# Kernel optimization log

Measured on AMD Instinct MI355X. Metric: run time of the kernel, lower is better.

## Reference

```python
import jax, jax.numpy as jnp
import numpy as np

D, E, K, H = 512, 8, 2, 128   # input_dim, num_experts, top-k, expert hidden (Expert default)
CAPF = 1.25                    # capacity_factor
N = 32768                      # tokens


def setup_inputs() -> dict:
    key = jax.random.key(0)
    ks = jax.random.split(key, 6)
    s = 0.02
    return {
        "x":  jax.random.normal(ks[0], (N, D), jnp.float32),
        "Wr": jax.random.normal(ks[1], (D, E), jnp.float32) * s,   # router linear weight
        "br": jnp.zeros((E,), jnp.float32),
        "W1": jax.random.normal(ks[2], (E, D, H), jnp.float32) * s,  # expert first linear (stacked)
        "b1": jnp.zeros((E, H), jnp.float32),
        "W2": jax.random.normal(ks[3], (E, H, D), jnp.float32) * s,  # expert second linear (stacked)
        "b2": jnp.zeros((E, D), jnp.float32),
    }


def reference(x, Wr, br, W1, b1, W2, b2):
    n = x.shape[0]
    # ---- router (eval mode: no noise, temperature=1) ----
    logits = x @ Wr + br                                   # [N, E]
    topk_vals, topk_idx = jax.lax.top_k(logits, K)         # [N, K]
    gates_k = jax.nn.softmax(topk_vals, axis=-1)
    rows = jnp.arange(n)[:, None]
    sparse_gates = jnp.zeros_like(logits).at[rows, topk_idx].set(gates_k)  # [N, E]
    confidence = topk_vals.max(axis=-1).mean()
    # ---- capacity-limited dispatch (keep first `cap` routed tokens per expert) ----
    cap = int(CAPF * (n / E))
    mask = sparse_gates > 0                                # [N, E] routed mask
    pos = jnp.cumsum(mask, axis=0) - 1                     # rank of token within expert queue
    keep = mask & (pos < cap)                              # [N, E]
    load = keep.sum(axis=0).astype(x.dtype)                # [E]
    # ---- per-expert 2-layer FFN over all tokens, combined with keep mask ----
    # (original adds expert output un-weighted by gates to kept token positions)
    h = jax.nn.relu(jnp.einsum('nd,edh->enh', x, W1) + b1[:, None, :])   # [E, N, H]
    y = jnp.einsum('enh,ehd->end', h, W2) + b2[:, None, :]               # [E, N, D]
    out = jnp.einsum('ne,end->nd', keep.astype(x.dtype), y)             # [N, D]
    # ---- load-balance stats ----
    load_dist = load / (load.sum() + 1e-8)
    load_loss = (load_dist * jnp.log(load_dist + 1e-8)).sum()
    return out, load_loss, load_dist, confidence
```

## Files before the change

kernel.cpp:

```cpp
#include <hip/hip_runtime.h>

#define D 512
#define E 8
#define H 128
#define BM 128
#define HP 136
#define RT 8

typedef __attribute__((ext_vector_type(8))) short short8v;
typedef __attribute__((ext_vector_type(4))) short short4v;
typedef __attribute__((ext_vector_type(4))) float float4v;

__device__ inline short f2bf(float f) {
  union { float f; unsigned u; } v; v.f = f;
  unsigned r = v.u + 0x7fffu + ((v.u >> 16) & 1u);
  return (short)(r >> 16);
}
__device__ inline float bf2f(short s) {
  union { unsigned u; float f; } v;
  v.u = ((unsigned)(unsigned short)s) << 16;
  return v.f;
}
__device__ inline void gload_lds4(const void* g, void* l) {
  __builtin_amdgcn_global_load_lds(
      (const __attribute__((address_space(1))) unsigned int*)g,
      (__attribute__((address_space(3))) unsigned int*)l, 4, 0, 0);
}

__global__ void k_swizzle(const float* __restrict__ W1, const float* __restrict__ W2,
                          short* __restrict__ W1f, short* __restrict__ W2f) {
  const int e = blockIdx.y;
  const int lane = threadIdx.x & 63;
  const int wv = threadIdx.x >> 6;
  const int r = lane & 15, g = lane >> 4;
  const int which = blockIdx.x >> 4;
  const int fbase = ((blockIdx.x & 15) * 4 + wv) * 2;
  if (which == 0) {
#pragma unroll
    for (int f = fbase; f < fbase + 2; ++f) {
      int ks = f >> 3, t = f & 7;
      const float* src = W1 + ((size_t)e * D + ks * 32 + g * 8) * H + t * 16 + r;
      short8v o;
#pragma unroll
      for (int j = 0; j < 8; ++j) o[j] = f2bf(src[(size_t)j * H]);
      *(short8v*)(W1f + (((size_t)e * 128 + f) * 64 + lane) * 8) = o;
    }
  } else {
#pragma unroll
    for (int f = fbase; f < fbase + 2; ++f) {
      int t = f >> 2, ks = f & 3;
      const float* src = W2 + ((size_t)e * H + ks * 32 + g * 8) * D + t * 16 + r;
      short8v o;
#pragma unroll
      for (int j = 0; j < 8; ++j) o[j] = f2bf(src[(size_t)j * D]);
      *(short8v*)(W2f + (((size_t)e * 128 + f) * 64 + lane) * 8) = o;
    }
  }
}

__global__ void k_router(const float* __restrict__ x, const float* __restrict__ Wr,
                         const float* __restrict__ br, int* __restrict__ tokE,
                         float* __restrict__ confPart, short* __restrict__ xb) {
  const int lane = threadIdx.x & 63;
  const int wave = threadIdx.x >> 6;
  const int tbase = (blockIdx.x * 4 + wave) * RT;

  float wr[8][8];
  const float4* wrp = reinterpret_cast<const float4*>(Wr) + lane * 16;
#pragma unroll
  for (int j = 0; j < 8; ++j) {
    float4 a = wrp[j * 2 + 0];
    float4 b = wrp[j * 2 + 1];
    wr[j][0] = a.x; wr[j][1] = a.y; wr[j][2] = a.z; wr[j][3] = a.w;
    wr[j][4] = b.x; wr[j][5] = b.y; wr[j][6] = b.z; wr[j][7] = b.w;
  }

  const int myE = ((lane & 1) << 2) | (lane & 2) | ((lane >> 2) & 1);
  const float brv = br[myE];

  float conf = 0.f;

#pragma unroll 2
  for (int tt = 0; tt < RT; ++tt) {
    const int token = tbase + tt;
    const float4* xp = reinterpret_cast<const float4*>(x + (size_t)token * D + lane * 8);
    float4 x0 = xp[0], x1 = xp[1];
    float xv[8] = {x0.x, x0.y, x0.z, x0.w, x1.x, x1.y, x1.z, x1.w};

    if (xb) {
      short8v p;
#pragma unroll
      for (int j = 0; j < 8; ++j) p[j] = f2bf(xv[j]);
      *(short8v*)(xb + (size_t)token * D + lane * 8) = p;
    }

    float v[8] = {0, 0, 0, 0, 0, 0, 0, 0};
#pragma unroll
    for (int j = 0; j < 8; ++j)
#pragma unroll
      for (int e = 0; e < E; ++e)
        v[e] += xv[j] * wr[j][e];

#pragma unroll
    for (int i = 0; i < 4; ++i) {
      float a = v[i] + __shfl_xor(v[i], 1, 64);
      float b = v[i + 4] + __shfl_xor(v[i + 4], 1, 64);
      v[i] = (lane & 1) ? b : a;
    }
#pragma unroll
    for (int i = 0; i < 2; ++i) {
      float a = v[i] + __shfl_xor(v[i], 2, 64);
      float b = v[i + 2] + __shfl_xor(v[i + 2], 2, 64);
      v[i] = (lane & 2) ? b : a;
    }
    {
      float a = v[0] + __shfl_xor(v[0], 4, 64);
      float b = v[1] + __shfl_xor(v[1], 4, 64);
      v[0] = (lane & 4) ? b : a;
    }
    v[0] += __shfl_xor(v[0], 8, 64);
    v[0] += __shfl_xor(v[0], 16, 64);
    v[0] += __shfl_xor(v[0], 32, 64);

    const float logit = v[0] + brv;

    float m1 = logit; int i1 = myE;
#pragma unroll
    for (int m = 1; m <= 4; m <<= 1) {
      float om = __shfl_xor(m1, m, 64);
      int oi = __shfl_xor(i1, m, 64);
      bool take = (om > m1) || (om == m1 && oi < i1);
      m1 = take ? om : m1;
      i1 = take ? oi : i1;
    }
    float s1 = (myE == i1) ? -1e30f : logit; int j1 = myE;
#pragma unroll
    for (int m = 1; m <= 4; m <<= 1) {
      float om = __shfl_xor(s1, m, 64);
      int oi = __shfl_xor(j1, m, 64);
      bool take = (om > s1) || (om == s1 && oi < j1);
      s1 = take ? om : s1;
      j1 = take ? oi : j1;
    }

    if (lane == 0) {
      tokE[token * 2 + 0] = i1;
      tokE[token * 2 + 1] = j1;
    }
    conf += m1;
  }

  __shared__ float cf[4];
  if (lane == 0) cf[wave] = conf;
  __syncthreads();
  if (threadIdx.x == 0) confPart[blockIdx.x] = cf[0] + cf[1] + cf[2] + cf[3];
}

__global__ void k_count(const int* __restrict__ tokE, int* __restrict__ chunkCnt) {
  __shared__ int c[E];
  if (threadIdx.x < E) c[threadIdx.x] = 0;
  __syncthreads();
  int token = blockIdx.x * 256 + threadIdx.x;
  atomicAdd(&c[tokE[token * 2 + 0]], 1);
  atomicAdd(&c[tokE[token * 2 + 1]], 1);
  __syncthreads();
  if (threadIdx.x < E) chunkCnt[blockIdx.x * E + threadIdx.x] = c[threadIdx.x];
}

__global__ void k_scan(const int* __restrict__ chunkCnt, const float* __restrict__ confPart,
                       int* __restrict__ chunkOff, int* __restrict__ kept,
                       float* __restrict__ outTail, int nConf, int cap, int nTok) {
  const int lane = threadIdx.x & 63;
  const int e = threadIdx.x >> 6;
  __shared__ int keptS[E];

  int v0 = chunkCnt[lane * E + e];
  int v1 = chunkCnt[(64 + lane) * E + e];
  int s0 = v0, s1 = v1;
#pragma unroll
  for (int off = 1; off < 64; off <<= 1) {
    int t0 = __shfl_up(s0, off, 64);
    int t1 = __shfl_up(s1, off, 64);
    if (lane >= off) { s0 += t0; s1 += t1; }
  }
  int tot0 = __shfl(s0, 63, 64);
  int total = tot0 + __shfl(s1, 63, 64);
  chunkOff[lane * E + e] = s0 - v0;
  chunkOff[(64 + lane) * E + e] = tot0 + s1 - v1;
  if (lane == 0) {
    int k = min(total, cap);
    kept[e] = k;
    keptS[e] = k;
  }

  __shared__ float s[512];
  float a = 0.f;
  for (int i = threadIdx.x; i < nConf; i += 512) a += confPart[i];
  s[threadIdx.x] = a;
  __syncthreads();
  for (int st = 256; st > 0; st >>= 1) {
    if (threadIdx.x < st) s[threadIdx.x] += s[threadIdx.x + st];
    __syncthreads();
  }
  if (threadIdx.x == 0) {
    float tot = 0.f, ld[E];
    for (int i = 0; i < E; ++i) { ld[i] = (float)keptS[i]; tot += ld[i]; }
    float denom = tot + 1e-8f;
    float loss = 0.f;
    for (int i = 0; i < E; ++i) {
      float dist = ld[i] / denom;
      loss += dist * logf(dist + 1e-8f);
      outTail[1 + i] = dist;
    }
    outTail[0] = loss;
    outTail[1 + E] = s[0] / (float)nTok;
  }
}

__global__ void k_dispatch(const int* __restrict__ tokE, const int* __restrict__ chunkOff,
                           int* __restrict__ expList, int2* __restrict__ tokSlot, int cap) {
  const int lane = threadIdx.x & 63;
  const int wave = threadIdx.x >> 6;
  const int token = blockIdx.x * 256 + threadIdx.x;
  const int e0 = tokE[token * 2 + 0];
  const int e1 = tokE[token * 2 + 1];
  __shared__ int wcnt[4][E];
  unsigned long long lt = (lane == 63) ? 0x7fffffffffffffffull : ((1ull << lane) - 1ull);
  int r0 = 0, r1 = 0;
#pragma unroll
  for (int e = 0; e < E; ++e) {
    unsigned long long b0 = __ballot(e0 == e);
    unsigned long long b1 = __ballot(e1 == e);
    unsigned long long m = b0 | b1;
    if (e0 == e) r0 = __popcll(m & lt);
    if (e1 == e) r1 = __popcll(m & lt);
    if (lane == 0) wcnt[wave][e] = __popcll(m);
  }
  __syncthreads();
  int base0 = chunkOff[blockIdx.x * E + e0];
  int base1 = chunkOff[blockIdx.x * E + e1];
  for (int w = 0; w < wave; ++w) {
    base0 += wcnt[w][e0];
    base1 += wcnt[w][e1];
  }
  int g0 = base0 + r0;
  int g1 = base1 + r1;
  if (g0 < cap) expList[e0 * cap + g0] = token;
  if (g1 < cap) expList[e1 * cap + g1] = token;
  tokSlot[token] = make_int2(g0 < cap ? e0 * cap + g0 : -1,
                             g1 < cap ? e1 * cap + g1 : -1);
}

template <bool USE_XB>
__global__ __launch_bounds__(512, 1) void k_expert_mfma(
    const short* __restrict__ xb, const float* __restrict__ x,
    const short* __restrict__ W1f, const float* __restrict__ b1,
    const short* __restrict__ W2f, const float* __restrict__ b2,
    const int* __restrict__ expList, const int* __restrict__ kept,
    short* __restrict__ yscr, int cap) {
  const int e = blockIdx.y;
  const int cnt = kept[e];
  const int t0 = blockIdx.x * BM;
  if (t0 >= cnt) return;
  const int lane = threadIdx.x & 63;
  const int wave = threadIdx.x >> 6;
  const int rowg = wave >> 2;
  const int ng = wave & 3;
  const int n15 = lane & 15;
  const int grp = lane >> 4;
  const int kg = grp * 8;

  __shared__ int toks[BM];
  __shared__ short sbuf[2 * BM * HP];

  if (threadIdx.x < BM) {
    int idx = min(t0 + (int)threadIdx.x, cnt - 1);
    toks[threadIdx.x] = expList[e * cap + idx];
  }
  __syncthreads();

  const short* w1 = W1f + (size_t)e * (128 * 512);
  const short* w2 = W2f + (size_t)e * (128 * 512);

  float4v acc[4][2];
#pragma unroll
  for (int r = 0; r < 4; ++r)
#pragma unroll
    for (int t = 0; t < 2; ++t)
      acc[r][t] = (float4v){0.f, 0.f, 0.f, 0.f};

  if (USE_XB) {
    auto stageX = [&](int p) {
#pragma unroll
      for (int j = 0; j < 16; ++j) {
        int ti = wave * 16 + j;
        const short* src = xb + (size_t)toks[ti] * D + p * 128 + lane * 2;
        short* dst = &sbuf[(p & 1) * (BM * HP) + ti * HP];
        gload_lds4(src, dst);
      }
    };
    stageX(0);
    __syncthreads();
#pragma unroll
    for (int p = 0; p < 4; ++p) {
      if (p < 3) stageX(p + 1);
#pragma unroll
      for (int ksl = 0; ksl < 4; ++ksl) {
        const int ks = p * 4 + ksl;
        const short* sb = &sbuf[(p & 1) * (BM * HP)];
        short8v xf[4];
#pragma unroll
        for (int r = 0; r < 4; ++r)
          xf[r] = *(const short8v*)&sb[(rowg * 64 + r * 16 + n15) * HP + ksl * 32 + kg];
        short8v wf[2];
#pragma unroll
        for (int t = 0; t < 2; ++t)
          wf[t] = *(const short8v*)(w1 + (size_t)(ks * 8 + ng * 2 + t) * 512 + lane * 8);
#pragma unroll
        for (int t = 0; t < 2; ++t)
#pragma unroll
          for (int r = 0; r < 4; ++r)
            acc[r][t] = __builtin_amdgcn_mfma_f32_16x16x32_bf16(wf[t], xf[r], acc[r][t], 0, 0, 0);
      }
      __syncthreads();
    }
  } else {
#pragma unroll 1
    for (int ks = 0; ks < 16; ++ks) {
      short8v xf[4];
#pragma unroll
      for (int r = 0; r < 4; ++r) {
        const float* xr = x + (size_t)toks[rowg * 64 + r * 16 + n15] * D + kg + ks * 32;
        float4 a0 = *(const float4*)(xr);
        float4 a1 = *(const float4*)(xr + 4);
        short8v f;
        f[0] = f2bf(a0.x); f[1] = f2bf(a0.y); f[2] = f2bf(a0.z); f[3] = f2bf(a0.w);
        f[4] = f2bf(a1.x); f[5] = f2bf(a1.y); f[6] = f2bf(a1.z); f[7] = f2bf(a1.w);
        xf[r] = f;
      }
      short8v wf[2];
#pragma unroll
      for (int t = 0; t < 2; ++t)
        wf[t] = *(const short8v*)(w1 + (size_t)(ks * 8 + ng * 2 + t) * 512 + lane * 8);
#pragma unroll
      for (int t = 0; t < 2; ++t)
#pragma unroll
        for (int r = 0; r < 4; ++r)
          acc[r][t] = __builtin_amdgcn_mfma_f32_16x16x32_bf16(wf[t], xf[r], acc[r][t], 0, 0, 0);
    }
    __syncthreads();
  }

#pragma unroll
  for (int t = 0; t < 2; ++t) {
    int tg = ng * 2 + t;
    float4 bb = *(const float4*)(b1 + e * H + tg * 16 + grp * 4);
#pragma unroll
    for (int r = 0; r < 4; ++r) {
      short4v p;
      p[0] = f2bf(fmaxf(acc[r][t][0] + bb.x, 0.f));
      p[1] = f2bf(fmaxf(acc[r][t][1] + bb.y, 0.f));
      p[2] = f2bf(fmaxf(acc[r][t][2] + bb.z, 0.f));
      p[3] = f2bf(fmaxf(acc[r][t][3] + bb.w, 0.f));
      *(short4v*)(&sbuf[(rowg * 64 + r * 16 + n15) * HP + tg * 16 + grp * 4]) = p;
    }
  }
  __syncthreads();

#pragma unroll
  for (int rp = 0; rp < 2; ++rp) {
    const int rbase = rowg * 64 + rp * 32;
    short8v a4[2][4];
#pragma unroll
    for (int ri = 0; ri < 2; ++ri)
#pragma unroll
      for (int ks = 0; ks < 4; ++ks)
        a4[ri][ks] = *(const short8v*)(&sbuf[(rbase + ri * 16 + n15) * HP + ks * 32 + kg]);

    short* yrow0 = yscr + ((size_t)(e * cap + t0 + rbase + n15)) * D;
    short* yrow1 = yrow0 + (size_t)16 * D;
#pragma unroll 4
    for (int tt = 0; tt < 8; ++tt) {
      const int t = ng * 8 + tt;
      short8v wf[4];
#pragma unroll
      for (int ks = 0; ks < 4; ++ks)
        wf[ks] = *(const short8v*)(w2 + (size_t)(t * 4 + ks) * 512 + lane * 8);
      float4v y0 = (float4v){0.f, 0.f, 0.f, 0.f};
      float4v y1 = (float4v){0.f, 0.f, 0.f, 0.f};
#pragma unroll
      for (int ks = 0; ks < 4; ++ks) {
        y0 = __builtin_amdgcn_mfma_f32_16x16x32_bf16(wf[ks], a4[0][ks], y0, 0, 0, 0);
        y1 = __builtin_amdgcn_mfma_f32_16x16x32_bf16(wf[ks], a4[1][ks], y1, 0, 0, 0);
      }
      float4 bb = *(const float4*)(b2 + e * D + t * 16 + grp * 4);
      short4v p0, p1;
      p0[0] = f2bf(y0[0] + bb.x);
      p0[1] = f2bf(y0[1] + bb.y);
      p0[2] = f2bf(y0[2] + bb.z);
      p0[3] = f2bf(y0[3] + bb.w);
      p1[0] = f2bf(y1[0] + bb.x);
      p1[1] = f2bf(y1[1] + bb.y);
      p1[2] = f2bf(y1[2] + bb.z);
      p1[3] = f2bf(y1[3] + bb.w);
      *(short4v*)(yrow0 + t * 16 + grp * 4) = p0;
      *(short4v*)(yrow1 + t * 16 + grp * 4) = p1;
    }
  }
}

__global__ void k_combine(const short* __restrict__ yscr, const int2* __restrict__ tokSlot,
                          float* __restrict__ out) {
  const int idx = blockIdx.x * 256 + threadIdx.x;
  const int token = idx >> 7;
  const int c4 = idx & 127;
  int2 sl = tokSlot[token];
  float4 r = make_float4(0.f, 0.f, 0.f, 0.f);
  if (sl.x >= 0) {
    short4v y = *(const short4v*)(yscr + (size_t)sl.x * D + c4 * 4);
    r.x += bf2f(y[0]); r.y += bf2f(y[1]); r.z += bf2f(y[2]); r.w += bf2f(y[3]);
  }
  if (sl.y >= 0) {
    short4v y = *(const short4v*)(yscr + (size_t)sl.y * D + c4 * 4);
    r.x += bf2f(y[0]); r.y += bf2f(y[1]); r.z += bf2f(y[2]); r.w += bf2f(y[3]);
  }
  reinterpret_cast<float4*>(out)[idx] = r;
}

extern "C" void kernel_launch(void* const* d_in, const int* in_sizes, int n_in,
                              void* d_out, int out_size, void* d_ws, size_t ws_size,
                              hipStream_t stream) {
  const float* x  = (const float*)d_in[0];
  const float* Wr = (const float*)d_in[1];
  const float* br = (const float*)d_in[2];
  const float* W1 = (const float*)d_in[3];
  const float* b1 = (const float*)d_in[4];
  const float* W2 = (const float*)d_in[5];
  const float* b2 = (const float*)d_in[6];
  float* out = (float*)d_out;

  const int N = in_sizes[0] / D;
  const int cap = (int)(1.25f * (float)(N / E));
  const int chunks = N / 256;
  const int rblocks = N / (4 * RT);

  int* tokE = (int*)d_ws;
  float* confPart = (float*)(tokE + (size_t)N * 2);
  int* chunkCnt = (int*)(confPart + rblocks);
  int* chunkOff = chunkCnt + chunks * E;
  int* kept = chunkOff + chunks * E;
  int2* tokSlot = (int2*)(kept + E);
  int* expList = (int*)(tokSlot + N);
  short* W1f = (short*)(expList + (size_t)E * cap);
  short* W2f = W1f + (size_t)E * H * D;
  short* yscr = W2f + (size_t)E * H * D;
  short* xb = yscr + (size_t)E * cap * D;

  const size_t needed = (size_t)((char*)(xb + (size_t)N * D) - (char*)d_ws);
  const bool useXB = ws_size >= needed;

  k_swizzle<<<dim3(32, E), 256, 0, stream>>>(W1, W2, W1f, W2f);

  k_router<<<rblocks, 256, 0, stream>>>(x, Wr, br, tokE, confPart,
                                        useXB ? xb : nullptr);
  k_count<<<chunks, 256, 0, stream>>>(tokE, chunkCnt);
  k_scan<<<1, 512, 0, stream>>>(chunkCnt, confPart, chunkOff, kept,
                                out + (size_t)N * D, rblocks, cap, N);
  k_dispatch<<<chunks, 256, 0, stream>>>(tokE, chunkOff, expList, tokSlot, cap);

  const int tiles = (cap + BM - 1) / BM;
  dim3 g5(tiles, E);
  if (useXB)
    k_expert_mfma<true><<<g5, 512, 0, stream>>>(xb, x, W1f, b1, W2f, b2,
                                                expList, kept, yscr, cap);
  else
    k_expert_mfma<false><<<g5, 512, 0, stream>>>(nullptr, x, W1f, b1, W2f, b2,
                                                 expList, kept, yscr, cap);

  k_combine<<<(N * D / 4) / 256, 256, 0, stream>>>(yscr, tokSlot, out);
}
```

Baseline: 105.5 us.

## Replace LDS-staged double-buffered x gather with direct register loads

Removes the global_load_lds double-buffered staging of gathered bf16 token rows and instead loads each lane's x fragments straight from global memory into registers, with precomputed row pointers and a fully unrolled K loop. LDS shrinks to a single hidden-activation buffer and the launch bound no longer pins one block per SM, which could allow higher occupancy. The cost is losing the explicit prefetch overlap and the coalesced row staging, so the first GEMM may become more latency-bound on scattered gathers.

```diff
diff --git a/kernel.cpp b/kernel.cpp
--- a/kernel.cpp
+++ b/kernel.cpp
@@ -20,11 +20,6 @@
   union { unsigned u; float f; } v;
   v.u = ((unsigned)(unsigned short)s) << 16;
   return v.f;
-}
-__device__ inline void gload_lds4(const void* g, void* l) {
-  __builtin_amdgcn_global_load_lds(
-      (const __attribute__((address_space(1))) unsigned int*)g,
-      (__attribute__((address_space(3))) unsigned int*)l, 4, 0, 0);
 }
 
 __global__ void k_swizzle(const float* __restrict__ W1, const float* __restrict__ W2,
@@ -252,7 +247,7 @@
 }
 
 template <bool USE_XB>
-__global__ __launch_bounds__(512, 1) void k_expert_mfma(
+__global__ __launch_bounds__(512) void k_expert_mfma(
     const short* __restrict__ xb, const float* __restrict__ x,
     const short* __restrict__ W1f, const float* __restrict__ b1,
     const short* __restrict__ W2f, const float* __restrict__ b2,
@@ -271,7 +266,7 @@
   const int kg = grp * 8;
 
   __shared__ int toks[BM];
-  __shared__ short sbuf[2 * BM * HP];
+  __shared__ short hs[BM][HP];
 
   if (threadIdx.x < BM) {
     int idx = min(t0 + (int)threadIdx.x, cnt - 1);
@@ -282,6 +277,15 @@
   const short* w1 = W1f + (size_t)e * (128 * 512);
   const short* w2 = W2f + (size_t)e * (128 * 512);
 
+  const short* xrB[4];
+  const float* xrF[4];
+#pragma unroll
+  for (int r = 0; r < 4; ++r) {
+    int row = toks[rowg * 64 + r * 16 + n15];
+    if (USE_XB) xrB[r] = xb + (size_t)row * D + kg;
+    else        xrF[r] = x + (size_t)row * D + kg;
+  }
+
   float4v acc[4][2];
 #pragma unroll
   for (int r = 0; r < 4; ++r)
@@ -289,66 +293,33 @@
     for (int t = 0; t < 2; ++t)
       acc[r][t] = (float4v){0.f, 0.f, 0.f, 0.f};
 
-  if (USE_XB) {
-    auto stageX = [&](int p) {
-#pragma unroll
-      for (int j = 0; j < 16; ++j) {
-        int ti = wave * 16 + j;
-        const short* src = xb + (size_t)toks[ti] * D + p * 128 + lane * 2;
-        short* dst = &sbuf[(p & 1) * (BM * HP) + ti * HP];
-        gload_lds4(src, dst);
-      }
-    };
-    stageX(0);
-    __syncthreads();
-#pragma unroll
-    for (int p = 0; p < 4; ++p) {
-      if (p < 3) stageX(p + 1);
-#pragma unroll
-      for (int ksl = 0; ksl < 4; ++ksl) {
-        const int ks = p * 4 + ksl;
-        const short* sb = &sbuf[(p & 1) * (BM * HP)];
-        short8v xf[4];
-#pragma unroll
-        for (int r = 0; r < 4; ++r)
-          xf[r] = *(const short8v*)&sb[(rowg * 64 + r * 16 + n15) * HP + ksl * 32 + kg];
-        short8v wf[2];
-#pragma unroll
-        for (int t = 0; t < 2; ++t)
-          wf[t] = *(const short8v*)(w1 + (size_t)(ks * 8 + ng * 2 + t) * 512 + lane * 8);
-#pragma unroll
-        for (int t = 0; t < 2; ++t)
-#pragma unroll
-          for (int r = 0; r < 4; ++r)
-            acc[r][t] = __builtin_amdgcn_mfma_f32_16x16x32_bf16(wf[t], xf[r], acc[r][t], 0, 0, 0);
-      }
-      __syncthreads();
-    }
-  } else {
-#pragma unroll 1
-    for (int ks = 0; ks < 16; ++ks) {
-      short8v xf[4];
+#pragma unroll
+  for (int ks = 0; ks < 16; ++ks) {
+    short8v xf[4];
+    if (USE_XB) {
+#pragma unroll
+      for (int r = 0; r < 4; ++r)
+        xf[r] = *(const short8v*)(xrB[r] + ks * 32);
+    } else {
 #pragma unroll
       for (int r = 0; r < 4; ++r) {
-        const float* xr = x + (size_t)toks[rowg * 64 + r * 16 + n15] * D + kg + ks * 32;
-        float4 a0 = *(const float4*)(xr);
-        float4 a1 = *(const float4*)(xr + 4);
+        float4 a0 = *(const float4*)(xrF[r] + ks * 32);
+        float4 a1 = *(const float4*)(xrF[r] + ks * 32 + 4);
         short8v f;
         f[0] = f2bf(a0.x); f[1] = f2bf(a0.y); f[2] = f2bf(a0.z); f[3] = f2bf(a0.w);
         f[4] = f2bf(a1.x); f[5] = f2bf(a1.y); f[6] = f2bf(a1.z); f[7] = f2bf(a1.w);
         xf[r] = f;
       }
-      short8v wf[2];
-#pragma unroll
-      for (int t = 0; t < 2; ++t)
-        wf[t] = *(const short8v*)(w1 + (size_t)(ks * 8 + ng * 2 + t) * 512 + lane * 8);
-#pragma unroll
-      for (int t = 0; t < 2; ++t)
-#pragma unroll
-        for (int r = 0; r < 4; ++r)
-          acc[r][t] = __builtin_amdgcn_mfma_f32_16x16x32_bf16(wf[t], xf[r], acc[r][t], 0, 0, 0);
-    }
-    __syncthreads();
+    }
+    short8v wf[2];
+#pragma unroll
+    for (int t = 0; t < 2; ++t)
+      wf[t] = *(const short8v*)(w1 + (size_t)(ks * 8 + ng * 2 + t) * 512 + lane * 8);
+#pragma unroll
+    for (int t = 0; t < 2; ++t)
+#pragma unroll
+      for (int r = 0; r < 4; ++r)
+        acc[r][t] = __builtin_amdgcn_mfma_f32_16x16x32_bf16(wf[t], xf[r], acc[r][t], 0, 0, 0);
   }
 
 #pragma unroll
@@ -362,7 +333,7 @@
       p[1] = f2bf(fmaxf(acc[r][t][1] + bb.y, 0.f));
       p[2] = f2bf(fmaxf(acc[r][t][2] + bb.z, 0.f));
       p[3] = f2bf(fmaxf(acc[r][t][3] + bb.w, 0.f));
-      *(short4v*)(&sbuf[(rowg * 64 + r * 16 + n15) * HP + tg * 16 + grp * 4]) = p;
+      *(short4v*)(&hs[rowg * 64 + r * 16 + n15][tg * 16 + grp * 4]) = p;
     }
   }
   __syncthreads();
@@ -375,7 +346,7 @@
     for (int ri = 0; ri < 2; ++ri)
 #pragma unroll
       for (int ks = 0; ks < 4; ++ks)
-        a4[ri][ks] = *(const short8v*)(&sbuf[(rbase + ri * 16 + n15) * HP + ks * 32 + kg]);
+        a4[ri][ks] = *(const short8v*)(&hs[rbase + ri * 16 + n15][ks * 32 + kg]);
 
     short* yrow0 = yscr + ((size_t)(e * cap + t0 + rbase + n15)) * D;
     short* yrow1 = yrow0 + (size_t)16 * D;
```

Result: slower. 126.1 us (+19.5%).

## Prefetch expert weight fragments and reuse W2 loads across all row tiles

Applied to the files above, without the earlier changes.

In the first expert GEMM, each phase now loads all X fragments from LDS up front and prefetches the next k-slice of W1 from global memory into registers one step ahead. In the second GEMM, the two-pass row loop becomes a single pass over all four 16-row tiles, so each W2 fragment is loaded once instead of twice, again with next-step prefetching. The aim is to hide global weight-load latency behind MFMA work and halve W2 global traffic. The cost is higher register pressure, which may lower occupancy or cause spills.

```diff
diff --git a/kernel.cpp b/kernel.cpp
--- a/kernel.cpp
+++ b/kernel.cpp
@@ -281,6 +281,7 @@
 
   const short* w1 = W1f + (size_t)e * (128 * 512);
   const short* w2 = W2f + (size_t)e * (128 * 512);
+  const short* w1p = w1 + (size_t)(ng * 2) * 512 + lane * 8;
 
   float4v acc[4][2];
 #pragma unroll
@@ -304,23 +305,30 @@
 #pragma unroll
     for (int p = 0; p < 4; ++p) {
       if (p < 3) stageX(p + 1);
+      const short* sb = &sbuf[(p & 1) * (BM * HP)];
+      short8v xf[4][4];
+#pragma unroll
+      for (int ksl = 0; ksl < 4; ++ksl)
+#pragma unroll
+        for (int r = 0; r < 4; ++r)
+          xf[ksl][r] = *(const short8v*)&sb[(rowg * 64 + r * 16 + n15) * HP + ksl * 32 + kg];
+      const short* wp = w1p + (size_t)(p * 4) * 8 * 512;
+      short8v wc0 = *(const short8v*)(wp);
+      short8v wc1 = *(const short8v*)(wp + 512);
 #pragma unroll
       for (int ksl = 0; ksl < 4; ++ksl) {
-        const int ks = p * 4 + ksl;
-        const short* sb = &sbuf[(p & 1) * (BM * HP)];
-        short8v xf[4];
+        short8v wn0 = wc0, wn1 = wc1;
+        if (ksl < 3) {
+          wn0 = *(const short8v*)(wp + (size_t)(ksl + 1) * 8 * 512);
+          wn1 = *(const short8v*)(wp + (size_t)(ksl + 1) * 8 * 512 + 512);
+        }
 #pragma unroll
         for (int r = 0; r < 4; ++r)
-          xf[r] = *(const short8v*)&sb[(rowg * 64 + r * 16 + n15) * HP + ksl * 32 + kg];
-        short8v wf[2];
-#pragma unroll
-        for (int t = 0; t < 2; ++t)
-          wf[t] = *(const short8v*)(w1 + (size_t)(ks * 8 + ng * 2 + t) * 512 + lane * 8);
-#pragma unroll
-        for (int t = 0; t < 2; ++t)
-#pragma unroll
-          for (int r = 0; r < 4; ++r)
-            acc[r][t] = __builtin_amdgcn_mfma_f32_16x16x32_bf16(wf[t], xf[r], acc[r][t], 0, 0, 0);
+          acc[r][0] = __builtin_amdgcn_mfma_f32_16x16x32_bf16(wc0, xf[ksl][r], acc[r][0], 0, 0, 0);
+#pragma unroll
+        for (int r = 0; r < 4; ++r)
+          acc[r][1] = __builtin_amdgcn_mfma_f32_16x16x32_bf16(wc1, xf[ksl][r], acc[r][1], 0, 0, 0);
+        wc0 = wn0; wc1 = wn1;
       }
       __syncthreads();
     }
@@ -338,15 +346,13 @@
         f[4] = f2bf(a1.x); f[5] = f2bf(a1.y); f[6] = f2bf(a1.z); f[7] = f2bf(a1.w);
         xf[r] = f;
       }
-      short8v wf[2];
-#pragma unroll
-      for (int t = 0; t < 2; ++t)
-        wf[t] = *(const short8v*)(w1 + (size_t)(ks * 8 + ng * 2 + t) * 512 + lane * 8);
-#pragma unroll
-      for (int t = 0; t < 2; ++t)
-#pragma unroll
-        for (int r = 0; r < 4; ++r)
-          acc[r][t] = __builtin_amdgcn_mfma_f32_16x16x32_bf16(wf[t], xf[r], acc[r][t], 0, 0, 0);
+      short8v wf0 = *(const short8v*)(w1p + (size_t)ks * 8 * 512);
+      short8v wf1 = *(const short8v*)(w1p + (size_t)ks * 8 * 512 + 512);
+#pragma unroll
+      for (int r = 0; r < 4; ++r) {
+        acc[r][0] = __builtin_amdgcn_mfma_f32_16x16x32_bf16(wf0, xf[r], acc[r][0], 0, 0, 0);
+        acc[r][1] = __builtin_amdgcn_mfma_f32_16x16x32_bf16(wf1, xf[r], acc[r][1], 0, 0, 0);
+      }
     }
     __syncthreads();
   }
@@ -367,45 +373,47 @@
   }
   __syncthreads();
 
-#pragma unroll
-  for (int rp = 0; rp < 2; ++rp) {
-    const int rbase = rowg * 64 + rp * 32;
-    short8v a4[2][4];
-#pragma unroll
-    for (int ri = 0; ri < 2; ++ri)
-#pragma unroll
-      for (int ks = 0; ks < 4; ++ks)
-        a4[ri][ks] = *(const short8v*)(&sbuf[(rbase + ri * 16 + n15) * HP + ks * 32 + kg]);
-
-    short* yrow0 = yscr + ((size_t)(e * cap + t0 + rbase + n15)) * D;
-    short* yrow1 = yrow0 + (size_t)16 * D;
-#pragma unroll 4
-    for (int tt = 0; tt < 8; ++tt) {
-      const int t = ng * 8 + tt;
-      short8v wf[4];
-#pragma unroll
-      for (int ks = 0; ks < 4; ++ks)
-        wf[ks] = *(const short8v*)(w2 + (size_t)(t * 4 + ks) * 512 + lane * 8);
-      float4v y0 = (float4v){0.f, 0.f, 0.f, 0.f};
-      float4v y1 = (float4v){0.f, 0.f, 0.f, 0.f};
-#pragma unroll
-      for (int ks = 0; ks < 4; ++ks) {
-        y0 = __builtin_amdgcn_mfma_f32_16x16x32_bf16(wf[ks], a4[0][ks], y0, 0, 0, 0);
-        y1 = __builtin_amdgcn_mfma_f32_16x16x32_bf16(wf[ks], a4[1][ks], y1, 0, 0, 0);
-      }
-      float4 bb = *(const float4*)(b2 + e * D + t * 16 + grp * 4);
-      short4v p0, p1;
-      p0[0] = f2bf(y0[0] + bb.x);
-      p0[1] = f2bf(y0[1] + bb.y);
-      p0[2] = f2bf(y0[2] + bb.z);
-      p0[3] = f2bf(y0[3] + bb.w);
-      p1[0] = f2bf(y1[0] + bb.x);
-      p1[1] = f2bf(y1[1] + bb.y);
-      p1[2] = f2bf(y1[2] + bb.z);
-      p1[3] = f2bf(y1[3] + bb.w);
-      *(short4v*)(yrow0 + t * 16 + grp * 4) = p0;
-      *(short4v*)(yrow1 + t * 16 + grp * 4) = p1;
-    }
+  short8v a4[4][4];
+#pragma unroll
+  for (int ri = 0; ri < 4; ++ri)
+#pragma unroll
+    for (int ks = 0; ks < 4; ++ks)
+      a4[ri][ks] = *(const short8v*)(&sbuf[(rowg * 64 + ri * 16 + n15) * HP + ks * 32 + kg]);
+
+  const short* w2p = w2 + (size_t)(ng * 8 * 4) * 512 + lane * 8;
+  short* yr0 = yscr + ((size_t)(e * cap + t0 + rowg * 64 + n15)) * D;
+
+  short8v wc0 = *(const short8v*)(w2p + 0 * 512);
+  short8v wc1 = *(const short8v*)(w2p + 1 * 512);
+  short8v wc2 = *(const short8v*)(w2p + 2 * 512);
+  short8v wc3 = *(const short8v*)(w2p + 3 * 512);
+#pragma unroll
+  for (int tt = 0; tt < 8; ++tt) {
+    short8v wn0 = wc0, wn1 = wc1, wn2 = wc2, wn3 = wc3;
+    if (tt < 7) {
+      const short* np = w2p + (size_t)(tt + 1) * 4 * 512;
+      wn0 = *(const short8v*)(np + 0 * 512);
+      wn1 = *(const short8v*)(np + 1 * 512);
+      wn2 = *(const short8v*)(np + 2 * 512);
+      wn3 = *(const short8v*)(np + 3 * 512);
+    }
+    const int t = ng * 8 + tt;
+    float4 bb = *(const float4*)(b2 + e * D + t * 16 + grp * 4);
+#pragma unroll
+    for (int ri = 0; ri < 4; ++ri) {
+      float4v y = (float4v){0.f, 0.f, 0.f, 0.f};
+      y = __builtin_amdgcn_mfma_f32_16x16x32_bf16(wc0, a4[ri][0], y, 0, 0, 0);
+      y = __builtin_amdgcn_mfma_f32_16x16x32_bf16(wc1, a4[ri][1], y, 0, 0, 0);
+      y = __builtin_amdgcn_mfma_f32_16x16x32_bf16(wc2, a4[ri][2], y, 0, 0, 0);
+      y = __builtin_amdgcn_mfma_f32_16x16x32_bf16(wc3, a4[ri][3], y, 0, 0, 0);
+      short4v pv;
+      pv[0] = f2bf(y[0] + bb.x);
+      pv[1] = f2bf(y[1] + bb.y);
+      pv[2] = f2bf(y[2] + bb.z);
+      pv[3] = f2bf(y[3] + bb.w);
+      *(short4v*)(yr0 + (size_t)ri * 16 * D + t * 16 + grp * 4) = pv;
+    }
+    wc0 = wn0; wc1 = wn1; wc2 = wn2; wc3 = wn3;
   }
 }
 
```

After: 107.5 us. About the same (+1.9%).
